# Optimization experiments

Hardware: AMD Instinct MI355X
Metric: run time of the kernel (lower is better)

## Reference

```python
import jax, jax.numpy as jnp
import numpy as np

B, CIN, SEQ, H, W = 16, 8, 32, 128, 128
COUT, K = 8, 3


def setup_inputs() -> dict:
    key = jax.random.key(0)
    k1, k2, k3 = jax.random.split(key, 3)
    X = jax.random.normal(k1, (B, CIN, SEQ, H, W), dtype=jnp.float32)
    # single gate conv: [4*Cout, Cin+Cout, K, K]
    Wc = jax.random.normal(k2, (4 * COUT, CIN + COUT, K, K), dtype=jnp.float32) * 0.05
    bc = jax.random.normal(k3, (4 * COUT,), dtype=jnp.float32) * 0.05
    return {"X": X, "Wc": Wc, "bc": bc}


def reference(X, Wc, bc):
    # X: (B, Cin, S, H, W) -> cell_output: (B, Cout, S, H, W)
    Bb, Cin, S, Hh, Ww = X.shape
    Cout = Wc.shape[0] // 4
    h0 = jnp.zeros((Bb, Cout, Hh, Ww), X.dtype)
    c0 = jnp.zeros_like(h0)
    Xt = jnp.moveaxis(X, 2, 0)  # (S, B, Cin, H, W) for scan over time

    def step(carry, x):
        h, c = carry
        z = jax.lax.conv_general_dilated(
            jnp.concatenate([x, h], axis=1), Wc,
            window_strides=(1, 1), padding=((1, 1), (1, 1)),
            dimension_numbers=("NCHW", "OIHW", "NCHW"),
        ) + bc[None, :, None, None]
        i, f, g, o = jnp.split(z, 4, axis=1)
        c_new = jax.nn.sigmoid(f) * c + jax.nn.sigmoid(i) * jnp.tanh(g)
        h_new = jax.nn.sigmoid(o) * jnp.tanh(c_new)
        return (h_new, c_new), h_new

    _, hs = jax.lax.scan(step, (h0, c0), Xt)  # hs: (S, B, Cout, H, W)
    return jnp.moveaxis(hs, 0, 2)  # (B, Cout, S, H, W)
```

## Files before the change

kernel.cpp:

```cpp
#include <hip/hip_runtime.h>

#define SEQ   32
#define HH    128
#define WW    128
#define CINC  8
#define COUTC 8
#define NG    32
#define ICH   16
#define TAPS  9
#define ROWS  4
#define COLS  130

typedef _Float16 half8 __attribute__((ext_vector_type(8)));
typedef _Float16 half4 __attribute__((ext_vector_type(4)));
typedef float floatx16 __attribute__((ext_vector_type(16)));

__device__ __forceinline__ float fast_rcp(float x) { return __builtin_amdgcn_rcpf(x); }
__device__ __forceinline__ float sigmoidf_(float x) {
    return fast_rcp(1.0f + __expf(-x));
}
__device__ __forceinline__ float tanhf_(float x) {
    float e = __expf(-2.0f * x);
    return (1.0f - e) * fast_rcp(1.0f + e);
}

__global__ void prep_weights(const float* __restrict__ Wc, _Float16* __restrict__ Wf,
                             unsigned* __restrict__ flags) {
    int i = blockIdx.x * 256 + threadIdx.x;
    if (i < 1024) flags[i] = 0u;
    if (i >= TAPS * NG * ICH) return;
    int tap = i / (NG * ICH);
    int r   = i % (NG * ICH);
    int g   = r >> 4;
    int ch  = r & 15;
    int half = ch >> 3, c8 = ch & 7;
    int ky = tap / 3, kx = tap % 3;
    float w = Wc[g * (ICH * 9) + ch * 9 + ky * 3 + kx];
    Wf[((tap * NG + g) * 2 + half) * 8 + c8] = (_Float16)w;
}

__global__ __launch_bounds__(256, 4) void lstm_fused(
    const float* __restrict__ X,
    const _Float16* __restrict__ Wf,
    const float* __restrict__ bc,
    float* __restrict__ out,
    unsigned* __restrict__ flags)
{
    __shared__ __align__(16) _Float16 ldsH[2 * ROWS * COLS * 8];
    __shared__ __align__(16) _Float16 ldsL[2 * ROWS * COLS * 8];

    const int tid = threadIdx.x;
    const int blk = blockIdx.x;
    const int b   = blk >> 6;
    const int yb  = blk & 63;
    const int y0  = yb * 2;

    const int lane = tid & 63;
    const int w    = tid >> 6;
    const int lg   = lane & 31;
    const int lh   = lane >> 5;

    const bool hasUp = (yb > 0);
    const bool hasDn = (yb < 63);

    half8 wfrag[TAPS];
#pragma unroll
    for (int tap = 0; tap < TAPS; ++tap)
        wfrag[tap] = *(const half8*)&Wf[((tap * NG + lg) * 2 + lh) * 8];

    float bi[4], bf4[4], bg[4], bo[4];
#pragma unroll
    for (int r = 0; r < 4; ++r) {
        int oc = r + 4 * lh;
        bi[r]  = bc[oc];
        bf4[r] = bc[oc + 8];
        bg[r]  = bc[oc + 16];
        bo[r]  = bc[oc + 24];
    }

    float creg[8];
#pragma unroll
    for (int r = 0; r < 8; ++r) creg[r] = 0.0f;

    const int ry = w >> 1;
    const int x0 = (w & 1) * 64;
    const int y  = y0 + ry;

    for (int t = 0; t < SEQ; ++t) {
        if (t > 0) {
            if (tid == 0 && hasUp) {
                int polls = 0;
                while (__hip_atomic_fetch_add(&flags[blk - 1], 0u, __ATOMIC_RELAXED,
                                              __HIP_MEMORY_SCOPE_AGENT) < (unsigned)t
                       && ++polls < 100000)
                    __builtin_amdgcn_s_sleep(2);
            }
            if (tid == 64 && hasDn) {
                int polls = 0;
                while (__hip_atomic_fetch_add(&flags[blk + 1], 0u, __ATOMIC_RELAXED,
                                              __HIP_MEMORY_SCOPE_AGENT) < (unsigned)t
                       && ++polls < 100000)
                    __builtin_amdgcn_s_sleep(2);
            }
            __syncthreads();
        }

        for (int idx = tid; idx < 2 * ROWS * COLS; idx += 256) {
            int col  = idx % COLS;
            int tmp  = idx / COLS;
            int half = tmp >> 2;
            int row  = tmp & 3;
            if (half == 1 && t > 0 && (row == 1 || row == 2)) continue;
            int gy = y0 + row - 1;
            int gx = col - 1;
            bool inb = ((unsigned)gy < HH) && ((unsigned)gx < WW);
            float v[8];
#pragma unroll
            for (int j = 0; j < 8; ++j) {
                float val = 0.0f;
                if (half == 0) {
                    if (inb)
                        val = X[(((size_t)(b * CINC + j) * SEQ + t) * HH + gy) * WW + gx];
                } else {
                    if (inb && t > 0)
                        val = __hip_atomic_load(
                            &out[(((size_t)(b * COUTC + j) * SEQ + (t - 1)) * HH + gy) * WW + gx],
                            __ATOMIC_RELAXED, __HIP_MEMORY_SCOPE_AGENT);
                }
                v[j] = val;
            }
            union { half8 h; float4 f; } uh, ul;
#pragma unroll
            for (int j = 0; j < 8; ++j) {
                _Float16 hi = (_Float16)v[j];
                uh.h[j] = hi;
                ul.h[j] = (_Float16)(v[j] - (float)hi);
            }
            *(float4*)&ldsH[(size_t)idx * 8] = uh.f;
            *(float4*)&ldsL[(size_t)idx * 8] = ul.f;
        }
        __syncthreads();

        floatx16 acc0, acc1;
#pragma unroll
        for (int r = 0; r < 16; ++r) { acc0[r] = 0.0f; acc1[r] = 0.0f; }

#pragma unroll
        for (int tap = 0; tap < TAPS; ++tap) {
            int ky = tap / 3, kx = tap % 3;
            int row = ry + ky;
            int base0 = ((lh * ROWS + row) * COLS + (x0 + lg + kx)) * 8;
            int base1 = base0 + 32 * 8;
            half8 bh0 = *(const half8*)&ldsH[base0];
            half8 bl0 = *(const half8*)&ldsL[base0];
            half8 bh1 = *(const half8*)&ldsH[base1];
            half8 bl1 = *(const half8*)&ldsL[base1];
            acc0 = __builtin_amdgcn_mfma_f32_32x32x16_f16(wfrag[tap], bh0, acc0, 0, 0, 0);
            acc1 = __builtin_amdgcn_mfma_f32_32x32x16_f16(wfrag[tap], bh1, acc1, 0, 0, 0);
            acc0 = __builtin_amdgcn_mfma_f32_32x32x16_f16(wfrag[tap], bl0, acc0, 0, 0, 0);
            acc1 = __builtin_amdgcn_mfma_f32_32x32x16_f16(wfrag[tap], bl1, acc1, 0, 0, 0);
        }
        __syncthreads();

#pragma unroll
        for (int tl = 0; tl < 2; ++tl) {
            floatx16 A = tl ? acc1 : acc0;
            int px = x0 + tl * 32 + lg;
            half4 hh, hl;
#pragma unroll
            for (int r = 0; r < 4; ++r) {
                int oc = r + 4 * lh;
                float zi = A[r]      + bi[r];
                float zf = A[4 + r]  + bf4[r];
                float zg = A[8 + r]  + bg[r];
                float zo = A[12 + r] + bo[r];
                float cp = creg[tl * 4 + r];
                float cn = sigmoidf_(zf) * cp + sigmoidf_(zi) * tanhf_(zg);
                creg[tl * 4 + r] = cn;
                float hval = sigmoidf_(zo) * tanhf_(cn);
                __hip_atomic_store(
                    &out[(((size_t)(b * COUTC + oc) * SEQ + t) * HH + y) * WW + px],
                    hval, __ATOMIC_RELAXED, __HIP_MEMORY_SCOPE_AGENT);
                _Float16 hi = (_Float16)hval;
                hh[r] = hi;
                hl[r] = (_Float16)(hval - (float)hi);
            }
            int hbase = (((1 * ROWS) + 1 + ry) * COLS + (px + 1)) * 8 + 4 * lh;
            *(half4*)&ldsH[hbase] = hh;
            *(half4*)&ldsL[hbase] = hl;
        }

        __syncthreads();
        if (tid == 0 && t + 1 < SEQ)
            __hip_atomic_fetch_add(&flags[blk], 1u,
                                   __ATOMIC_RELAXED, __HIP_MEMORY_SCOPE_AGENT);
    }
}

__global__ __launch_bounds__(256, 4) void step_kernel(
    const float* __restrict__ X,
    const _Float16* __restrict__ Wf,
    const float* __restrict__ bc,
    float* __restrict__ out,
    float* __restrict__ c,
    int t)
{
    __shared__ __align__(16) _Float16 ldsH[2 * ROWS * COLS * 8];
    __shared__ __align__(16) _Float16 ldsL[2 * ROWS * COLS * 8];

    const int tid = threadIdx.x;
    const int b   = blockIdx.x >> 6;
    const int y0  = (blockIdx.x & 63) * 2;

    for (int idx = tid; idx < 2 * ROWS * COLS; idx += 256) {
        int col  = idx % COLS;
        int tmp  = idx / COLS;
        int half = tmp >> 2;
        int row  = tmp & 3;
        int gy = y0 + row - 1;
        int gx = col - 1;
        bool inb = ((unsigned)gy < HH) && ((unsigned)gx < WW);
        float v[8];
#pragma unroll
        for (int j = 0; j < 8; ++j) {
            int ch = half * 8 + j;
            float val = 0.0f;
            if (inb) {
                if (ch < CINC)
                    val = X[(((size_t)(b * CINC + ch) * SEQ + t) * HH + gy) * WW + gx];
                else if (t > 0)
                    val = out[(((size_t)(b * COUTC + (ch - 8)) * SEQ + (t - 1)) * HH + gy) * WW + gx];
            }
            v[j] = val;
        }
        union { half8 h; float4 f; } uh, ul;
#pragma unroll
        for (int j = 0; j < 8; ++j) {
            _Float16 hi = (_Float16)v[j];
            uh.h[j] = hi;
            ul.h[j] = (_Float16)(v[j] - (float)hi);
        }
        *(float4*)&ldsH[(size_t)idx * 8] = uh.f;
        *(float4*)&ldsL[(size_t)idx * 8] = ul.f;
    }

    const int lane = tid & 63;
    const int w    = tid >> 6;
    const int lg   = lane & 31;
    const int lh   = lane >> 5;

    half8 wfrag[TAPS];
#pragma unroll
    for (int tap = 0; tap < TAPS; ++tap)
        wfrag[tap] = *(const half8*)&Wf[((tap * NG + lg) * 2 + lh) * 8];

    __syncthreads();

    const int ry = w >> 1;
    const int x0 = (w & 1) * 64;

    floatx16 acc0, acc1;
#pragma unroll
    for (int r = 0; r < 16; ++r) { acc0[r] = 0.0f; acc1[r] = 0.0f; }

#pragma unroll
    for (int tap = 0; tap < TAPS; ++tap) {
        int ky = tap / 3, kx = tap % 3;
        int row = ry + ky;
        int base0 = ((lh * ROWS + row) * COLS + (x0 + lg + kx)) * 8;
        int base1 = base0 + 32 * 8;
        half8 bh0 = *(const half8*)&ldsH[base0];
        half8 bl0 = *(const half8*)&ldsL[base0];
        half8 bh1 = *(const half8*)&ldsH[base1];
        half8 bl1 = *(const half8*)&ldsL[base1];
        acc0 = __builtin_amdgcn_mfma_f32_32x32x16_f16(wfrag[tap], bh0, acc0, 0, 0, 0);
        acc1 = __builtin_amdgcn_mfma_f32_32x32x16_f16(wfrag[tap], bh1, acc1, 0, 0, 0);
        acc0 = __builtin_amdgcn_mfma_f32_32x32x16_f16(wfrag[tap], bl0, acc0, 0, 0, 0);
        acc1 = __builtin_amdgcn_mfma_f32_32x32x16_f16(wfrag[tap], bl1, acc1, 0, 0, 0);
    }

    const int y = y0 + ry;
#pragma unroll
    for (int tl = 0; tl < 2; ++tl) {
        floatx16 A = tl ? acc1 : acc0;
        int px = x0 + tl * 32 + lg;
#pragma unroll
        for (int r = 0; r < 4; ++r) {
            int oc = r + 4 * lh;
            float zi = A[r]      + bc[oc];
            float zf = A[4 + r]  + bc[oc + 8];
            float zg = A[8 + r]  + bc[oc + 16];
            float zo = A[12 + r] + bc[oc + 24];
            size_t ci = ((size_t)(b * COUTC + oc) * HH + y) * WW + px;
            float cp = (t > 0) ? c[ci] : 0.0f;
            float cn = sigmoidf_(zf) * cp + sigmoidf_(zi) * tanhf_(zg);
            c[ci] = cn;
            out[(((size_t)(b * COUTC + oc) * SEQ + t) * HH + y) * WW + px]
                = sigmoidf_(zo) * tanhf_(cn);
        }
    }
}

extern "C" void kernel_launch(void* const* d_in, const int* in_sizes, int n_in,
                              void* d_out, int out_size, void* d_ws, size_t ws_size,
                              hipStream_t stream) {
    const float* X  = (const float*)d_in[0];
    const float* Wc = (const float*)d_in[1];
    const float* bc = (const float*)d_in[2];
    float* out = (float*)d_out;

    _Float16* Wf    = (_Float16*)d_ws;
    unsigned* flags = (unsigned*)((char*)d_ws + 12288);

    prep_weights<<<18, 256, 0, stream>>>(Wc, Wf, flags);

    void* args[] = { (void*)&X, (void*)&Wf, (void*)&bc, (void*)&out, (void*)&flags };
    hipError_t err = hipLaunchCooperativeKernel((const void*)lstm_fused,
                                                dim3(16 * 64), dim3(256),
                                                args, 0, stream);
    if (err != hipSuccess) {
        float* c = (float*)((char*)d_ws + 16384);
        for (int t = 0; t < SEQ; ++t) {
            step_kernel<<<16 * 64, 256, 0, stream>>>(X, Wf, bc, out, c, t);
        }
    }
}
```

Baseline: 854.6 us.

## Overlap halo wait with partial MFMA taps and prefetch next-step input

The timestep loop is restructured so waves 0 and 1 poll the neighbour flags and stage only the single halo row each needs. Waves 2 and 3 meanwhile compute the taps that do not depend on the halo rows (taps 0-5 for the lower row). The X tile for the next timestep is staged right after the flag is published, moving input loading off the critical dependency chain. This aims to hide inter-block synchronisation latency, at the cost of uneven wave work and an extra barrier per step.

```diff
diff --git a/kernel.cpp b/kernel.cpp
--- a/kernel.cpp
+++ b/kernel.cpp
@@ -39,6 +39,81 @@
     Wf[((tap * NG + g) * 2 + half) * 8 + c8] = (_Float16)w;
 }
 
+__device__ __forceinline__ void stage_X(const float* __restrict__ X, int b, int y0, int tt,
+                                        int tid, _Float16* ldsH, _Float16* ldsL) {
+#pragma unroll
+    for (int i = 0; i < 3; ++i) {
+        int idx = tid + i * 256;
+        if (idx >= ROWS * COLS) break;
+        int col = idx % COLS;
+        int row = idx / COLS;
+        int gy = y0 + row - 1;
+        int gx = col - 1;
+        bool inb = ((unsigned)gy < HH) && ((unsigned)gx < WW);
+        float v[8];
+#pragma unroll
+        for (int j = 0; j < 8; ++j)
+            v[j] = inb ? X[(((size_t)(b * CINC + j) * SEQ + tt) * HH + gy) * WW + gx] : 0.0f;
+        union { half8 h; float4 f; } uh, ul;
+#pragma unroll
+        for (int j = 0; j < 8; ++j) {
+            _Float16 hi = (_Float16)v[j];
+            uh.h[j] = hi;
+            ul.h[j] = (_Float16)(v[j] - (float)hi);
+        }
+        *(float4*)&ldsH[(size_t)idx * 8] = uh.f;
+        *(float4*)&ldsL[(size_t)idx * 8] = ul.f;
+    }
+}
+
+__device__ __forceinline__ void stage_halo(const float* __restrict__ out, int b, int gy,
+                                           int t, int ldsrow, int lane,
+                                           _Float16* ldsH, _Float16* ldsL) {
+    for (int col = lane; col < COLS; col += 64) {
+        int gx = col - 1;
+        bool inb = ((unsigned)gy < HH) && ((unsigned)gx < WW);
+        float v[8];
+#pragma unroll
+        for (int j = 0; j < 8; ++j)
+            v[j] = inb ? __hip_atomic_load(
+                             &out[(((size_t)(b * COUTC + j) * SEQ + (t - 1)) * HH + gy) * WW + gx],
+                             __ATOMIC_RELAXED, __HIP_MEMORY_SCOPE_AGENT)
+                       : 0.0f;
+        union { half8 h; float4 f; } uh, ul;
+#pragma unroll
+        for (int j = 0; j < 8; ++j) {
+            _Float16 hi = (_Float16)v[j];
+            uh.h[j] = hi;
+            ul.h[j] = (_Float16)(v[j] - (float)hi);
+        }
+        int item = ROWS * COLS + ldsrow * COLS + col;
+        *(float4*)&ldsH[(size_t)item * 8] = uh.f;
+        *(float4*)&ldsL[(size_t)item * 8] = ul.f;
+    }
+}
+
+template <int T0, int T1>
+__device__ __forceinline__ void do_taps(int ry, int x0, int lg, int lh,
+                                        const half8* wfrag,
+                                        const _Float16* ldsH, const _Float16* ldsL,
+                                        floatx16& acc0, floatx16& acc1) {
+#pragma unroll
+    for (int tap = T0; tap < T1; ++tap) {
+        int ky = tap / 3, kx = tap % 3;
+        int row = ry + ky;
+        int base0 = ((lh * ROWS + row) * COLS + (x0 + lg + kx)) * 8;
+        int base1 = base0 + 32 * 8;
+        half8 bh0 = *(const half8*)&ldsH[base0];
+        half8 bl0 = *(const half8*)&ldsL[base0];
+        half8 bh1 = *(const half8*)&ldsH[base1];
+        half8 bl1 = *(const half8*)&ldsL[base1];
+        acc0 = __builtin_amdgcn_mfma_f32_32x32x16_f16(wfrag[tap], bh0, acc0, 0, 0, 0);
+        acc1 = __builtin_amdgcn_mfma_f32_32x32x16_f16(wfrag[tap], bh1, acc1, 0, 0, 0);
+        acc0 = __builtin_amdgcn_mfma_f32_32x32x16_f16(wfrag[tap], bl0, acc0, 0, 0, 0);
+        acc1 = __builtin_amdgcn_mfma_f32_32x32x16_f16(wfrag[tap], bl1, acc1, 0, 0, 0);
+    }
+}
+
 __global__ __launch_bounds__(256, 4) void lstm_fused(
     const float* __restrict__ X,
     const _Float16* __restrict__ Wf,
@@ -86,80 +161,55 @@
     const int x0 = (w & 1) * 64;
     const int y  = y0 + ry;
 
+#pragma unroll
+    for (int i = 0; i < 3; ++i) {
+        int idx = tid + i * 256;
+        if (idx >= ROWS * COLS) break;
+        int item = ROWS * COLS + idx;
+        *(float4*)&ldsH[(size_t)item * 8] = float4{0.f, 0.f, 0.f, 0.f};
+        *(float4*)&ldsL[(size_t)item * 8] = float4{0.f, 0.f, 0.f, 0.f};
+    }
+    stage_X(X, b, y0, 0, tid, ldsH, ldsL);
+    __syncthreads();
+
     for (int t = 0; t < SEQ; ++t) {
-        if (t > 0) {
-            if (tid == 0 && hasUp) {
-                int polls = 0;
-                while (__hip_atomic_fetch_add(&flags[blk - 1], 0u, __ATOMIC_RELAXED,
-                                              __HIP_MEMORY_SCOPE_AGENT) < (unsigned)t
-                       && ++polls < 100000)
-                    __builtin_amdgcn_s_sleep(2);
+        floatx16 acc0, acc1;
+#pragma unroll
+        for (int r = 0; r < 16; ++r) { acc0[r] = 0.0f; acc1[r] = 0.0f; }
+
+        if (w == 0) {
+            if (t > 0) {
+                if (hasUp && lane == 0) {
+                    int polls = 0;
+                    while (__hip_atomic_fetch_add(&flags[blk - 1], 0u, __ATOMIC_RELAXED,
+                                                  __HIP_MEMORY_SCOPE_AGENT) < (unsigned)t
+                           && ++polls < (1 << 17))
+                        __builtin_amdgcn_s_sleep(1);
+                }
+                asm volatile("" ::: "memory");
+                stage_halo(out, b, y0 - 1, t, 0, lane, ldsH, ldsL);
             }
-            if (tid == 64 && hasDn) {
-                int polls = 0;
-                while (__hip_atomic_fetch_add(&flags[blk + 1], 0u, __ATOMIC_RELAXED,
-                                              __HIP_MEMORY_SCOPE_AGENT) < (unsigned)t
-                       && ++polls < 100000)
-                    __builtin_amdgcn_s_sleep(2);
+        } else if (w == 1) {
+            if (t > 0) {
+                if (hasDn && lane == 0) {
+                    int polls = 0;
+                    while (__hip_atomic_fetch_add(&flags[blk + 1], 0u, __ATOMIC_RELAXED,
+                                                  __HIP_MEMORY_SCOPE_AGENT) < (unsigned)t
+                           && ++polls < (1 << 17))
+                        __builtin_amdgcn_s_sleep(1);
+                }
+                asm volatile("" ::: "memory");
+                stage_halo(out, b, y0 + 2, t, 3, lane, ldsH, ldsL);
             }
-            __syncthreads();
-        }
-
-        for (int idx = tid; idx < 2 * ROWS * COLS; idx += 256) {
-            int col  = idx % COLS;
-            int tmp  = idx / COLS;
-            int half = tmp >> 2;
-            int row  = tmp & 3;
-            if (half == 1 && t > 0 && (row == 1 || row == 2)) continue;
-            int gy = y0 + row - 1;
-            int gx = col - 1;
-            bool inb = ((unsigned)gy < HH) && ((unsigned)gx < WW);
-            float v[8];
-#pragma unroll
-            for (int j = 0; j < 8; ++j) {
-                float val = 0.0f;
-                if (half == 0) {
-                    if (inb)
-                        val = X[(((size_t)(b * CINC + j) * SEQ + t) * HH + gy) * WW + gx];
-                } else {
-                    if (inb && t > 0)
-                        val = __hip_atomic_load(
-                            &out[(((size_t)(b * COUTC + j) * SEQ + (t - 1)) * HH + gy) * WW + gx],
-                            __ATOMIC_RELAXED, __HIP_MEMORY_SCOPE_AGENT);
-                }
-                v[j] = val;
-            }
-            union { half8 h; float4 f; } uh, ul;
-#pragma unroll
-            for (int j = 0; j < 8; ++j) {
-                _Float16 hi = (_Float16)v[j];
-                uh.h[j] = hi;
-                ul.h[j] = (_Float16)(v[j] - (float)hi);
-            }
-            *(float4*)&ldsH[(size_t)idx * 8] = uh.f;
-            *(float4*)&ldsL[(size_t)idx * 8] = ul.f;
+        } else {
+            do_taps<0, 6>(ry, x0, lg, lh, wfrag, ldsH, ldsL, acc0, acc1);
         }
         __syncthreads();
 
-        floatx16 acc0, acc1;
-#pragma unroll
-        for (int r = 0; r < 16; ++r) { acc0[r] = 0.0f; acc1[r] = 0.0f; }
-
-#pragma unroll
-        for (int tap = 0; tap < TAPS; ++tap) {
-            int ky = tap / 3, kx = tap % 3;
-            int row = ry + ky;
-            int base0 = ((lh * ROWS + row) * COLS + (x0 + lg + kx)) * 8;
-            int base1 = base0 + 32 * 8;
-            half8 bh0 = *(const half8*)&ldsH[base0];
-            half8 bl0 = *(const half8*)&ldsL[base0];
-            half8 bh1 = *(const half8*)&ldsH[base1];
-            half8 bl1 = *(const half8*)&ldsL[base1];
-            acc0 = __builtin_amdgcn_mfma_f32_32x32x16_f16(wfrag[tap], bh0, acc0, 0, 0, 0);
-            acc1 = __builtin_amdgcn_mfma_f32_32x32x16_f16(wfrag[tap], bh1, acc1, 0, 0, 0);
-            acc0 = __builtin_amdgcn_mfma_f32_32x32x16_f16(wfrag[tap], bl0, acc0, 0, 0, 0);
-            acc1 = __builtin_amdgcn_mfma_f32_32x32x16_f16(wfrag[tap], bl1, acc1, 0, 0, 0);
-        }
+        if (ry == 0)
+            do_taps<0, 9>(ry, x0, lg, lh, wfrag, ldsH, ldsL, acc0, acc1);
+        else
+            do_taps<6, 9>(ry, x0, lg, lh, wfrag, ldsH, ldsL, acc0, acc1);
         __syncthreads();
 
 #pragma unroll
@@ -194,6 +244,10 @@
         if (tid == 0 && t + 1 < SEQ)
             __hip_atomic_fetch_add(&flags[blk], 1u,
                                    __ATOMIC_RELAXED, __HIP_MEMORY_SCOPE_AGENT);
+
+        if (t + 1 < SEQ)
+            stage_X(X, b, y0, t + 1, tid, ldsH, ldsL);
+        __syncthreads();
     }
 }
 
```

After: 964.2 us. 12.8% more time.
